# Optimization experiments

Measured on AMD Instinct MI355X. Metric: run time of the kernel, lower is better.

The kernel has to match this reference:

```python
import jax, jax.numpy as jnp
import numpy as np

B, N, D = 16, 1024, 768
SCALE = D ** (-0.5)


def setup_inputs() -> dict:
    key = jax.random.key(0)
    ks = jax.random.split(key, 6)
    return {
        "x": jax.random.normal(ks[0], (B, N, D), dtype=jnp.float32),
        "y": jax.random.normal(ks[1], (B, N, D), dtype=jnp.float32),
        "coords": jax.random.normal(ks[2], (N, N, 6), dtype=jnp.float32),
        "W_qk": jax.random.normal(ks[3], (D, D), dtype=jnp.float32) * (D ** -0.5),
        "pos_emb": jax.random.normal(ks[4], (N, 6, 1), dtype=jnp.float32) * 0.02,
        "gating": jnp.float32(1.0),
        "temp": jnp.float32(0.1),
    }


def reference(x, y, coords, W_qk, pos_emb, gating, temp):
    # k = Linear(y), no bias; torch Linear: y @ W.T
    k = jnp.einsum('bnd,ed->bne', y, W_qk)
    # content score [B, N, N]
    patch_score = jax.nn.softmax(jnp.einsum('bnd,bmd->bnm', x, k) * SCALE, axis=-1)
    # positional score: coords [N, N, 6] @ pos_emb [N, 6, 1] -> [N, N]
    pos_score = jax.nn.softmax(jnp.einsum('pnk,pkl->pnl', coords, pos_emb)[..., 0], axis=-1)
    g = jax.nn.sigmoid(gating)
    attn = (1.0 - g) * patch_score + g * pos_score[None, :, :]  # broadcast over B
    out = jnp.einsum('bnm,bmd->bnd', attn, y)
    entropy = jnp.sum(-attn * jnp.log(attn + 1e-8), axis=-1, keepdims=True)  # [B, N, 1]
    hmap = 2.0 * (1.0 - jax.nn.sigmoid(temp * entropy))
    return out, hmap
```

## Files before the change

### kernel.cpp

```cpp
#include <hip/hip_runtime.h>
#include <hip/hip_bf16.h>
#include <cstdint>

typedef __bf16 bf16_t;
typedef __bf16 bf16x8 __attribute__((ext_vector_type(8)));
typedef __bf16 bf16x4 __attribute__((ext_vector_type(4)));
typedef float f32x4 __attribute__((ext_vector_type(4)));

static constexpr int B = 16, N = 1024, D = 768;
static constexpr float SCALE = 0.03608439182435161f;

#define ASYNC_COPY16(gptr, lptr)                                                          \
  __builtin_amdgcn_global_load_lds((const __attribute__((address_space(1))) void*)(gptr), \
                                   (__attribute__((address_space(3))) void*)(lptr), 16, 0, 0)

__device__ __forceinline__ float wave_red_max(float v) {
#pragma unroll
  for (int o = 32; o > 0; o >>= 1) v = fmaxf(v, __shfl_down(v, o, 64));
  return v;
}
__device__ __forceinline__ float wave_red_sum(float v) {
#pragma unroll
  for (int o = 32; o > 0; o >>= 1) v += __shfl_down(v, o, 64);
  return v;
}
__device__ __forceinline__ float block_max(float v, float* sm) {
  v = wave_red_max(v);
  int lane = threadIdx.x & 63, w = threadIdx.x >> 6;
  if (lane == 0) sm[w] = v;
  __syncthreads();
  return fmaxf(fmaxf(sm[0], sm[1]), fmaxf(sm[2], sm[3]));
}
__device__ __forceinline__ float block_sum(float v, float* sm) {
  v = wave_red_sum(v);
  int lane = threadIdx.x & 63, w = threadIdx.x >> 6;
  if (lane == 0) sm[w] = v;
  __syncthreads();
  return sm[0] + sm[1] + sm[2] + sm[3];
}

__global__ __launch_bounds__(256) void cast_f32_bf16_4(const float4* __restrict__ in,
                                                       bf16x4* __restrict__ out, int n4) {
  int i = blockIdx.x * 256 + threadIdx.x;
  if (i < n4) {
    float4 v = in[i];
    bf16x4 o;
    o.x = (bf16_t)v.x; o.y = (bf16_t)v.y; o.z = (bf16_t)v.z; o.w = (bf16_t)v.w;
    out[i] = o;
  }
}

__global__ __launch_bounds__(256) void transpose_bf16(const bf16_t* __restrict__ in,
                                                      bf16_t* __restrict__ out) {
  __shared__ bf16_t t[32][33];
  int b = blockIdx.z;
  int d0 = blockIdx.x * 32;
  int n0 = blockIdx.y * 32;
  int tx = threadIdx.x & 31;
  int ty = threadIdx.x >> 5;
  const bf16_t* src = in + (size_t)b * N * D;
  bf16_t* dst = out + (size_t)b * N * D;
#pragma unroll
  for (int r = 0; r < 4; r++) {
    int n = n0 + ty + r * 8;
    t[ty + r * 8][tx] = src[(size_t)n * D + d0 + tx];
  }
  __syncthreads();
#pragma unroll
  for (int r = 0; r < 4; r++) {
    int d = d0 + ty + r * 8;
    dst[(size_t)d * N + n0 + tx] = t[tx][ty + r * 8];
  }
}

__global__ __launch_bounds__(256) void pos_softmax_k(const float* __restrict__ coords,
                                                     const float* __restrict__ pemb,
                                                     float* __restrict__ pos) {
  __shared__ float sm1[4], sm2[4];
  int p = blockIdx.x;
  int tid = threadIdx.x;
  float e[6];
#pragma unroll
  for (int k = 0; k < 6; k++) e[k] = pemb[p * 6 + k];
  float v[4];
#pragma unroll
  for (int i = 0; i < 4; i++) {
    int n = tid + i * 256;
    const float* c = coords + ((size_t)p * N + n) * 6;
    float s = 0.f;
#pragma unroll
    for (int k = 0; k < 6; k++) s += c[k] * e[k];
    v[i] = s;
  }
  float m = block_max(fmaxf(fmaxf(v[0], v[1]), fmaxf(v[2], v[3])), sm1);
  float ex[4], ls = 0.f;
#pragma unroll
  for (int i = 0; i < 4; i++) { ex[i] = __expf(v[i] - m); ls += ex[i]; }
  float sum = block_sum(ls, sm2);
  float inv = 1.f / sum;
#pragma unroll
  for (int i = 0; i < 4; i++) pos[(size_t)p * N + tid + i * 256] = ex[i] * inv;
}

__global__ __launch_bounds__(256) void attn_entropy_k(float* __restrict__ S,
                                                      const float* __restrict__ pos,
                                                      const float* __restrict__ gating,
                                                      const float* __restrict__ temp,
                                                      float* __restrict__ hmap) {
  __shared__ float sm1[4], sm2[4], sm3[4];
  size_t row = blockIdx.x;
  int q = (int)(row & (size_t)(N - 1));
  int tid = threadIdx.x;
  float* Srow = S + row * N;
  float g = 1.f / (1.f + __expf(-gating[0]));
  float s[4];
#pragma unroll
  for (int i = 0; i < 4; i++) s[i] = Srow[tid + i * 256];
  float m = block_max(fmaxf(fmaxf(s[0], s[1]), fmaxf(s[2], s[3])), sm1);
  float e[4], ls = 0.f;
#pragma unroll
  for (int i = 0; i < 4; i++) { e[i] = __expf(s[i] - m); ls += e[i]; }
  float sum = block_sum(ls, sm2);
  float inv = 1.f / sum;
  const float* prow = pos + (size_t)q * N;
  float a[4], ent = 0.f;
#pragma unroll
  for (int i = 0; i < 4; i++) {
    float patch = e[i] * inv;
    float ps = prow[tid + i * 256];
    a[i] = (1.f - g) * patch + g * ps;
    ent += -a[i] * __logf(a[i] + 1e-8f);
  }
  float E = block_sum(ent, sm3);
  __syncthreads();
  bf16_t* arow = (bf16_t*)Srow;
#pragma unroll
  for (int i = 0; i < 4; i++) arow[tid + i * 256] = (bf16_t)a[i];
  if (tid == 0) hmap[row] = 2.f / (1.f + __expf(temp[0] * E));
}

template <typename OutT>
__global__ __launch_bounds__(256) void gemm_nt_128(const bf16_t* __restrict__ A, int lda, long long sA,
                                                   const bf16_t* __restrict__ Bm, int ldb, long long sB,
                                                   OutT* __restrict__ C, int ldc, long long sC,
                                                   int K, float scale) {
  __shared__ __align__(16) bf16_t As[128 * 32];
  __shared__ __align__(16) bf16_t Bs[128 * 32];
  const int tid = threadIdx.x;
  const int lane = tid & 63, wave = tid >> 6;
  const int wr = wave >> 1, wc = wave & 1;
  const int quad = lane >> 4, lr = lane & 15;
  const int tileN = blockIdx.x * 128, tileM = blockIdx.y * 128;
  A += (long long)blockIdx.z * sA + (long long)tileM * lda;
  Bm += (long long)blockIdx.z * sB + (long long)tileN * ldb;
  C += (long long)blockIdx.z * sC;

  const int srow0 = wave * 32 + (lane >> 2);
  const int scol = (lane & 3) * 8;

  f32x4 acc[4][4];
#pragma unroll
  for (int i = 0; i < 4; i++)
#pragma unroll
    for (int j = 0; j < 4; j++) acc[i][j] = (f32x4){0.f, 0.f, 0.f, 0.f};

  for (int kt = 0; kt < K; kt += 32) {
#pragma unroll
    for (int i = 0; i < 2; i++) {
      ASYNC_COPY16(A + (long long)(srow0 + i * 16) * lda + kt + scol,
                   &As[(wave * 32 + i * 16) * 32]);
      ASYNC_COPY16(Bm + (long long)(srow0 + i * 16) * ldb + kt + scol,
                   &Bs[(wave * 32 + i * 16) * 32]);
    }
    __syncthreads();
    bf16x8 af[4], bf[4];
#pragma unroll
    for (int i = 0; i < 4; i++) {
      af[i] = *(const bf16x8*)&As[(wr * 64 + i * 16 + lr) * 32 + quad * 8];
      bf[i] = *(const bf16x8*)&Bs[(wc * 64 + i * 16 + lr) * 32 + quad * 8];
    }
#pragma unroll
    for (int mi = 0; mi < 4; mi++)
#pragma unroll
      for (int nj = 0; nj < 4; nj++)
        acc[mi][nj] = __builtin_amdgcn_mfma_f32_16x16x32_bf16(af[mi], bf[nj], acc[mi][nj], 0, 0, 0);
    __syncthreads();
  }
#pragma unroll
  for (int mi = 0; mi < 4; mi++)
#pragma unroll
    for (int nj = 0; nj < 4; nj++)
#pragma unroll
      for (int r = 0; r < 4; r++) {
        int row = tileM + wr * 64 + mi * 16 + quad * 4 + r;
        int col = tileN + wc * 64 + nj * 16 + lr;
        C[(long long)row * ldc + col] = (OutT)(acc[mi][nj][r] * scale);
      }
}

extern "C" void kernel_launch(void* const* d_in, const int* in_sizes, int n_in,
                              void* d_out, int out_size, void* d_ws, size_t ws_size,
                              hipStream_t stream) {
  const float* x = (const float*)d_in[0];
  const float* y = (const float*)d_in[1];
  const float* coords = (const float*)d_in[2];
  const float* W = (const float*)d_in[3];
  const float* pemb = (const float*)d_in[4];
  const float* gating = (const float*)d_in[5];
  const float* temp = (const float*)d_in[6];
  float* out = (float*)d_out;
  float* hmap = out + (size_t)B * N * D;

  char* ws = (char*)d_ws;
  bf16_t* xb = (bf16_t*)(ws + 0);
  bf16_t* yb = (bf16_t*)(ws + 25165824);
  bf16_t* yT = (bf16_t*)(ws + 50331648);
  bf16_t* Wb = (bf16_t*)(ws + 75497472);
  bf16_t* kb = (bf16_t*)(ws + 76677120);
  float* pos = (float*)(ws + 101842944);
  float* S   = (float*)(ws + 106037248);

  const int BND = B * N * D;

  cast_f32_bf16_4<<<BND / 4 / 256, 256, 0, stream>>>((const float4*)x, (bf16x4*)xb, BND / 4);
  cast_f32_bf16_4<<<BND / 4 / 256, 256, 0, stream>>>((const float4*)y, (bf16x4*)yb, BND / 4);
  cast_f32_bf16_4<<<(D * D / 4 + 255) / 256, 256, 0, stream>>>((const float4*)W, (bf16x4*)Wb, D * D / 4);
  transpose_bf16<<<dim3(D / 32, N / 32, B), 256, 0, stream>>>(yb, yT);
  pos_softmax_k<<<N, 256, 0, stream>>>(coords, pemb, pos);

  gemm_nt_128<bf16_t><<<dim3(D / 128, (B * N) / 128, 1), 256, 0, stream>>>(
      yb, D, 0LL, Wb, D, 0LL, kb, D, 0LL, D, 1.0f);

  gemm_nt_128<float><<<dim3(N / 128, N / 128, B), 256, 0, stream>>>(
      xb, D, (long long)N * D, kb, D, (long long)N * D, S, N, (long long)N * N, D, SCALE);

  attn_entropy_k<<<B * N, 256, 0, stream>>>(S, pos, gating, temp, hmap);

  gemm_nt_128<float><<<dim3(D / 128, N / 128, B), 256, 0, stream>>>(
      (const bf16_t*)S, 2 * N, (long long)N * 2 * N, yT, N, (long long)N * D, out, D, (long long)N * D, N, 1.0f);
}
```

Before: 352.0 us.

## Deepen GEMM K-tile to 64 and stage epilogue through LDS for vector stores

The 128x128 bf16 MFMA GEMM now loads a K=64 slab per iteration, which halves the number of barrier pairs per K sweep. The epilogue stages each wave's accumulators through padded LDS and writes them to global memory as 16-byte vectors (f32x4 or bf16x8) instead of scattered scalar stores. This targets barrier overhead and uncoalesced output writes. In exchange, LDS use grows to about 34 KB, which may reduce occupancy, and the unpadded 64-wide tiles can cause LDS bank conflicts on the fragment reads.

```diff
diff --git a/kernel.cpp b/kernel.cpp
--- a/kernel.cpp
+++ b/kernel.cpp
@@ -144,8 +144,10 @@
                                                    const bf16_t* __restrict__ Bm, int ldb, long long sB,
                                                    OutT* __restrict__ C, int ldc, long long sC,
                                                    int K, float scale) {
-  __shared__ __align__(16) bf16_t As[128 * 32];
-  __shared__ __align__(16) bf16_t Bs[128 * 32];
+  __shared__ __align__(16) char lds_raw[4 * 32 * 68 * 4];
+  bf16_t* As = (bf16_t*)lds_raw;
+  bf16_t* Bs = (bf16_t*)(lds_raw + 16384);
+
   const int tid = threadIdx.x;
   const int lane = tid & 63, wave = tid >> 6;
   const int wr = wave >> 1, wc = wave & 1;
@@ -155,8 +157,8 @@
   Bm += (long long)blockIdx.z * sB + (long long)tileN * ldb;
   C += (long long)blockIdx.z * sC;
 
-  const int srow0 = wave * 32 + (lane >> 2);
-  const int scol = (lane & 3) * 8;
+  const bf16_t* ag = A + (long long)(wave * 32 + (lane >> 3)) * lda + (lane & 7) * 8;
+  const bf16_t* bg = Bm + (long long)(wave * 32 + (lane >> 3)) * ldb + (lane & 7) * 8;
 
   f32x4 acc[4][4];
 #pragma unroll
@@ -164,38 +166,69 @@
 #pragma unroll
     for (int j = 0; j < 4; j++) acc[i][j] = (f32x4){0.f, 0.f, 0.f, 0.f};
 
-  for (int kt = 0; kt < K; kt += 32) {
-#pragma unroll
-    for (int i = 0; i < 2; i++) {
-      ASYNC_COPY16(A + (long long)(srow0 + i * 16) * lda + kt + scol,
-                   &As[(wave * 32 + i * 16) * 32]);
-      ASYNC_COPY16(Bm + (long long)(srow0 + i * 16) * ldb + kt + scol,
-                   &Bs[(wave * 32 + i * 16) * 32]);
+  for (int kt = 0; kt < K; kt += 64) {
+#pragma unroll
+    for (int i = 0; i < 4; i++) {
+      ASYNC_COPY16(ag + (long long)i * 8 * lda + kt, &As[(wave * 32 + i * 8) * 64]);
+      ASYNC_COPY16(bg + (long long)i * 8 * ldb + kt, &Bs[(wave * 32 + i * 8) * 64]);
     }
     __syncthreads();
-    bf16x8 af[4], bf[4];
-#pragma unroll
-    for (int i = 0; i < 4; i++) {
-      af[i] = *(const bf16x8*)&As[(wr * 64 + i * 16 + lr) * 32 + quad * 8];
-      bf[i] = *(const bf16x8*)&Bs[(wc * 64 + i * 16 + lr) * 32 + quad * 8];
-    }
-#pragma unroll
-    for (int mi = 0; mi < 4; mi++)
+#pragma unroll
+    for (int kk = 0; kk < 2; kk++) {
+      bf16x8 af[4], bfr[4];
+#pragma unroll
+      for (int i = 0; i < 4; i++) {
+        af[i] = *(const bf16x8*)&As[(wr * 64 + i * 16 + lr) * 64 + kk * 32 + quad * 8];
+        bfr[i] = *(const bf16x8*)&Bs[(wc * 64 + i * 16 + lr) * 64 + kk * 32 + quad * 8];
+      }
+#pragma unroll
+      for (int mi = 0; mi < 4; mi++)
+#pragma unroll
+        for (int nj = 0; nj < 4; nj++)
+          acc[mi][nj] = __builtin_amdgcn_mfma_f32_16x16x32_bf16(af[mi], bfr[nj], acc[mi][nj], 0, 0, 0);
+    }
+    __syncthreads();
+  }
+
+  float* epi = (float*)lds_raw + wave * (32 * 68);
+#pragma unroll
+  for (int c = 0; c < 2; c++) {
+#pragma unroll
+    for (int m2 = 0; m2 < 2; m2++) {
+      int mi = c * 2 + m2;
 #pragma unroll
       for (int nj = 0; nj < 4; nj++)
-        acc[mi][nj] = __builtin_amdgcn_mfma_f32_16x16x32_bf16(af[mi], bf[nj], acc[mi][nj], 0, 0, 0);
-    __syncthreads();
-  }
-#pragma unroll
-  for (int mi = 0; mi < 4; mi++)
-#pragma unroll
-    for (int nj = 0; nj < 4; nj++)
-#pragma unroll
-      for (int r = 0; r < 4; r++) {
-        int row = tileM + wr * 64 + mi * 16 + quad * 4 + r;
-        int col = tileN + wc * 64 + nj * 16 + lr;
-        C[(long long)row * ldc + col] = (OutT)(acc[mi][nj][r] * scale);
+#pragma unroll
+        for (int r = 0; r < 4; r++) {
+          int lrow = m2 * 16 + quad * 4 + r;
+          epi[lrow * 68 + nj * 16 + lr] = acc[mi][nj][r] * scale;
+        }
+    }
+    if constexpr (sizeof(OutT) == 4) {
+#pragma unroll
+      for (int seg = 0; seg < 8; seg++) {
+        int lrow = seg * 4 + (lane >> 4);
+        f32x4 v = *(const f32x4*)&epi[lrow * 68 + (lane & 15) * 4];
+        long long grow = tileM + wr * 64 + c * 32 + lrow;
+        int gcol = tileN + wc * 64 + (lane & 15) * 4;
+        *(f32x4*)&C[grow * ldc + gcol] = v;
       }
+    } else {
+#pragma unroll
+      for (int seg = 0; seg < 4; seg++) {
+        int lrow = seg * 8 + (lane >> 3);
+        const float* p = &epi[lrow * 68 + (lane & 7) * 8];
+        f32x4 v0 = *(const f32x4*)&p[0];
+        f32x4 v1 = *(const f32x4*)&p[4];
+        bf16x8 o;
+#pragma unroll
+        for (int j = 0; j < 4; j++) { o[j] = (bf16_t)v0[j]; o[j + 4] = (bf16_t)v1[j]; }
+        long long grow = tileM + wr * 64 + c * 32 + lrow;
+        int gcol = tileN + wc * 64 + (lane & 7) * 8;
+        *(bf16x8*)&C[grow * ldc + gcol] = o;
+      }
+    }
+  }
 }
 
 extern "C" void kernel_launch(void* const* d_in, const int* in_sizes, int n_in,
```

Result: no change. 356.6 us (+1.3%).
